# Kernel optimization log

Measured on AMD Instinct MI355X. Metric: run time of the kernel, lower is better.

## Reference

```python
import jax, jax.numpy as jnp
import numpy as np

B, L = 1, 8
K = 1024  # number of learned offsets / gathered channels
FULL_RES = (32, 32, 32)
EPS = 1e-5


def _trilinear(vol, cx, cy, cz):
    """torch.grid_sample (5D, mode='bilinear', padding='zeros', align_corners=False).
    vol: (D,H,W); cx,cy,cz: arbitrary matching shapes, normalized coords in [-1,1]
    with x->W, y->H, z->D (torch convention)."""
    D, H, W = vol.shape
    vflat = vol.reshape(-1)
    ix = ((cx + 1.0) * W - 1.0) * 0.5
    iy = ((cy + 1.0) * H - 1.0) * 0.5
    iz = ((cz + 1.0) * D - 1.0) * 0.5
    x0f, y0f, z0f = jnp.floor(ix), jnp.floor(iy), jnp.floor(iz)
    fx, fy, fz = ix - x0f, iy - y0f, iz - z0f
    x0 = x0f.astype(jnp.int32)
    y0 = y0f.astype(jnp.int32)
    z0 = z0f.astype(jnp.int32)
    out = jnp.zeros_like(ix)
    for dz in (0, 1):
        wz = fz if dz else 1.0 - fz
        zi = z0 + dz
        for dy in (0, 1):
            wy = fy if dy else 1.0 - fy
            yi = y0 + dy
            for dx in (0, 1):
                wx = fx if dx else 1.0 - fx
                xi = x0 + dx
                valid = (xi >= 0) & (xi < W) & (yi >= 0) & (yi < H) & (zi >= 0) & (zi < D)
                idx = (jnp.clip(zi, 0, D - 1) * H + jnp.clip(yi, 0, H - 1)) * W + jnp.clip(xi, 0, W - 1)
                out = out + (wz * wy * wx) * jnp.where(valid, vflat[idx], 0.0)
    return out


def _affine_identity_grid(D, H, W):
    # F.affine_grid(eye(3,4), align_corners=False): voxel-center coords in [-1,1]
    xs = (2.0 * jnp.arange(W) + 1.0) / W - 1.0
    ys = (2.0 * jnp.arange(H) + 1.0) / H - 1.0
    zs = (2.0 * jnp.arange(D) + 1.0) / D - 1.0
    zg, yg, xg = jnp.meshgrid(zs, ys, xs, indexing="ij")
    return jnp.stack([xg, yg, zg], axis=-1).reshape(-1, 3)  # (D*H*W, 3), order (x,y,z)


def _bn(x, g, b):
    # training-mode BatchNorm3d on flattened-spatial layout x:(B,C,N)
    m = jnp.mean(x, axis=(0, 2), keepdims=True)
    v = jnp.var(x, axis=(0, 2), keepdims=True)
    return (x - m) * jax.lax.rsqrt(v + EPS) * g[None, :, None] + b[None, :, None]


def _lin(x, w):  # 1x1x1 Conv3d, no bias: x:(B,C,N), w:(O,C)
    return jnp.einsum("bcn,oc->bon", x, w)


def _forward(images, offset1, w1, g1, b1, w2, g2, b2,
             w3a, w3b, w3c, w3d, g3a, b3a, g3b, b3b, g3c, b3c, g3d, b3d, w4, b4):
    Bn, _, D, H, W = images.shape
    base = _affine_identity_grid(D, H, W)  # (N,3)
    vols = images[:, 0]  # (B,D,H,W)

    def gather(off):  # off:(K,3) -> (B,K,N)
        c = base[None, :, :] + off[:, None, :]  # (K,N,3)
        return jax.vmap(lambda v: _trilinear(v, c[..., 0], c[..., 1], c[..., 2]))(vols)

    # dual offset trilinear gathers, subtracted (Obelisk feature)
    x = gather(offset1[:, 0]) - gather(offset1[:, 1])  # (B,1024,N)

    # grouped 1x1 conv (groups=4): (B,4,256,N) x (4,64,256) -> (B,256,N)
    xg = x.reshape(Bn, 4, 256, -1)
    y = jnp.einsum("bgcn,goc->bgon", xg, w1).reshape(Bn, 256, -1)
    x1 = jax.nn.relu(_bn(y, g1, b1))
    x2 = _bn(_lin(x1, w2), g2, b2)
    x3a = jnp.concatenate([x2, jax.nn.relu(_lin(x2, w3a))], axis=1)
    x3b = jnp.concatenate([x3a, jax.nn.relu(_lin(_bn(x3a, g3a, b3a), w3b))], axis=1)
    x3c = jnp.concatenate([x3b, jax.nn.relu(_lin(_bn(x3b, g3b, b3b), w3c))], axis=1)
    x3d = jnp.concatenate([x3c, jax.nn.relu(_lin(_bn(x3c, g3c, b3c), w3d))], axis=1)
    x4 = _lin(_bn(x3d, g3d, b3d), w4) + b4[None, :, None]
    out = jax.nn.sigmoid(x4)
    # F.interpolate to full_res is an identity here (grid already at full res)
    return out.reshape(Bn, -1, D, H, W)


def setup_inputs() -> dict:
    key = jax.random.key(0)
    ks = jax.random.split(key, 16)
    D, H, W = FULL_RES
    f32 = jnp.float32
    inp = {
        "images": jax.random.normal(ks[0], (B, 1, D, H, W), f32),
        "offset1": jax.random.normal(ks[1], (K, 2, 3), f32) * 0.2,
        "w1": jax.random.normal(ks[2], (4, 64, 256), f32) * 0.05,
        "g1": jnp.ones((256,), f32), "b1": jnp.zeros((256,), f32),
        "w2": jax.random.normal(ks[3], (128, 256), f32) * 0.05,
        "g2": jnp.ones((128,), f32), "b2": jnp.zeros((128,), f32),
        "w3a": jax.random.normal(ks[4], (32, 128), f32) * 0.05,
        "w3b": jax.random.normal(ks[5], (32, 160), f32) * 0.05,
        "w3c": jax.random.normal(ks[6], (32, 192), f32) * 0.05,
        "w3d": jax.random.normal(ks[7], (32, 224), f32) * 0.05,
        "g3a": jnp.ones((160,), f32), "b3a": jnp.zeros((160,), f32),
        "g3b": jnp.ones((192,), f32), "b3b": jnp.zeros((192,), f32),
        "g3c": jnp.ones((224,), f32), "b3c": jnp.zeros((224,), f32),
        "g3d": jnp.ones((256,), f32), "b3d": jnp.zeros((256,), f32),
        "w4": jax.random.normal(ks[8], (L, 256), f32) * 0.05,
        "b4": jnp.zeros((L,), f32),
    }
    return inp


def reference(images, offset1, w1, g1, b1, w2, g2, b2,
              w3a, w3b, w3c, w3d, g3a, b3a, g3b, b3b, g3c, b3c, g3d, b3d, w4, b4):
    return _forward(images, offset1, w1, g1, b1, w2, g2, b2,
                    w3a, w3b, w3c, w3d, g3a, b3a, g3b, b3b, g3c, b3c, g3d, b3d, w4, b4)
```

## Files before the change

### kernel.cpp

```cpp
#include <hip/hip_runtime.h>
#include <math.h>

#define VOXN 32768

typedef __attribute__((ext_vector_type(8))) short bf16x8;
typedef __attribute__((ext_vector_type(4))) float f32x4;

constexpr int OFF_STATS_Y   = 0;
constexpr int OFF_STATS_X2P = 512;
constexpr int OFF_STATS_H   = 768;
constexpr int OFF_TPAR      = 1280;
constexpr int OFF_W1A       = 17664;
constexpr int OFF_W2A       = 83200;
constexpr int OFF_W3AT      = 115968;
constexpr int OFF_W3BT      = 120064;
constexpr int OFF_W3CT      = 125184;
constexpr int OFF_W3DT      = 131328;
constexpr int OFF_W4T       = 138496;
constexpr int OFF_YH        = 140544;
constexpr int OFF_C0A       = OFF_YH;
constexpr int OFF_PERM      = OFF_YH + 1024;
constexpr int OFF_X2P       = 8529152;
constexpr int OFF_PVOLB     = OFF_X2P;

#define FMA4(A, W, X) { (A).x = fmaf((W).x, (X), (A).x); (A).y = fmaf((W).y, (X), (A).y); \
                        (A).z = fmaf((W).z, (X), (A).z); (A).w = fmaf((W).w, (X), (A).w); }
#define RELU4(A) { (A).x = fmaxf((A).x, 0.f); (A).y = fmaxf((A).y, 0.f); \
                   (A).z = fmaxf((A).z, 0.f); (A).w = fmaxf((A).w, 0.f); }
#define ZERO4(A) float4 A; (A).x = 0.f; (A).y = 0.f; (A).z = 0.f; (A).w = 0.f;

#define BFLY(s, q) { s += __shfl_xor(s, 32, 64); q += __shfl_xor(q, 32, 64); \
                     s += __shfl_xor(s, 16, 64); q += __shfl_xor(q, 16, 64); \
                     s += __shfl_xor(s,  8, 64); q += __shfl_xor(q,  8, 64); \
                     s += __shfl_xor(s,  4, 64); q += __shfl_xor(q,  4, 64); \
                     s += __shfl_xor(s,  2, 64); q += __shfl_xor(q,  2, 64); \
                     s += __shfl_xor(s,  1, 64); q += __shfl_xor(q,  1, 64); }
#define STASH1(V, O) { float s_ = (V), q_ = (V) * (V); BFLY(s_, q_) \
                       if (lane == (O)) { ms = s_; mq = q_; } }
#define STASH4(A, O0) STASH1((A).x, (O0)+0) STASH1((A).y, (O0)+1) \
                      STASH1((A).z, (O0)+2) STASH1((A).w, (O0)+3)

__device__ __forceinline__ unsigned short f2bf(float f) {
  unsigned int u = __float_as_uint(f);
  u += 0x7FFFu + ((u >> 16) & 1u);
  return (unsigned short)(u >> 16);
}

__device__ __forceinline__ float corner(const float* __restrict__ im, int x, int y, int z) {
  if (x >= 33 && x < 65 && y >= 33 && y < 65 && z >= 33 && z < 65)
    return im[((z - 33) * 32 + (y - 33)) * 32 + (x - 33)];
  return 0.f;
}

__device__ __forceinline__ int tap_c0(const float* __restrict__ offset1, int k, int s) {
  float ox = fminf(fmaxf(offset1[k * 6 + s * 3 + 0] * 16.f, -1000.f), 1000.f);
  float oy = fminf(fmaxf(offset1[k * 6 + s * 3 + 1] * 16.f, -1000.f), 1000.f);
  float oz = fminf(fmaxf(offset1[k * 6 + s * 3 + 2] * 16.f, -1000.f), 1000.f);
  int sx = (int)floorf(ox), sy = (int)floorf(oy), sz = (int)floorf(oz);
  bool valid = (sx >= -33 && sx <= 32) && (sy >= -33 && sy <= 32) && (sz >= -33 && sz <= 32);
  if (!valid) { sx = sy = sz = 0; }
  return (sz + 33) * 9604 + (sy + 33) * 98 + (sx + 33);
}

__global__ void s0a_setup(const float* __restrict__ images, const float* __restrict__ offset1,
                          const float* __restrict__ w3a, const float* __restrict__ w3b,
                          const float* __restrict__ w3c, const float* __restrict__ w3d,
                          const float* __restrict__ w4, float* __restrict__ ws)
{
  const int idx = blockIdx.x * blockDim.x + threadIdx.x;
  const int stride = gridDim.x * blockDim.x;
  for (int i = idx; i < 1280; i += stride) ws[i] = 0.f;
  uint4* qq = (uint4*)(ws + OFF_PVOLB);
  for (int i = idx; i < 941192; i += stride) {
    int x = i % 98, t = i / 98, y = t % 98, z = t / 98;
    uint4 f; f.x = 0u; f.y = 0u; f.z = 0u; f.w = 0u;
    if (x >= 32 && x <= 64 && y >= 32 && y <= 64 && z >= 32 && z <= 64) {
      float c000 = corner(images, x, y, z),     c100 = corner(images, x+1, y, z);
      float c010 = corner(images, x, y+1, z),   c110 = corner(images, x+1, y+1, z);
      float c001 = corner(images, x, y, z+1),   c101 = corner(images, x+1, y, z+1);
      float c011 = corner(images, x, y+1, z+1), c111 = corner(images, x+1, y+1, z+1);
      f.x = (unsigned int)f2bf(c000) | ((unsigned int)f2bf(c100) << 16);
      f.y = (unsigned int)f2bf(c010) | ((unsigned int)f2bf(c110) << 16);
      f.z = (unsigned int)f2bf(c001) | ((unsigned int)f2bf(c101) << 16);
      f.w = (unsigned int)f2bf(c011) | ((unsigned int)f2bf(c111) << 16);
    }
    qq[i] = f;
  }
  int* c0a = (int*)(ws + OFF_C0A);
  for (int k = idx; k < 1024; k += stride) c0a[k] = tap_c0(offset1, k, 0);
  for (int i = idx; i < 4096;  i += stride) { int o = i & 31,  c = i >> 5; ws[OFF_W3AT + i] = w3a[o * 128 + c]; }
  for (int i = idx; i < 5120;  i += stride) { int o = i & 31,  c = i >> 5; ws[OFF_W3BT + i] = w3b[o * 160 + c]; }
  for (int i = idx; i < 6144;  i += stride) { int o = i & 31,  c = i >> 5; ws[OFF_W3CT + i] = w3c[o * 192 + c]; }
  for (int i = idx; i < 7168;  i += stride) { int o = i & 31,  c = i >> 5; ws[OFF_W3DT + i] = w3d[o * 224 + c]; }
  for (int i = idx; i < 2048;  i += stride) { int l = i & 7,   c = i >> 3; ws[OFF_W4T + i] = w4[l * 256 + c]; }
}

__global__ void s0b_rank(float* __restrict__ ws)
{
  const int idx = blockIdx.x * blockDim.x + threadIdx.x;
  if (idx >= 1024) return;
  const int g = idx >> 8, k = idx & 255;
  const int* c0a = (const int*)(ws + OFF_C0A);
  int* perm = (int*)(ws + OFF_PERM);
  const int my = c0a[g * 256 + k];
  int rank = 0;
  for (int j = 0; j < 256; ++j) {
    int cj = c0a[g * 256 + j];
    rank += (cj < my) || (cj == my && j < k);
  }
  perm[g * 256 + rank] = k;
}

__global__ void s0c_build(const float* __restrict__ offset1, const float* __restrict__ w1,
                          const float* __restrict__ w2, float* __restrict__ ws)
{
  const int idx = blockIdx.x * blockDim.x + threadIdx.x;
  const int stride = gridDim.x * blockDim.x;
  const int* perm = (const int*)(ws + OFF_PERM);
  for (int p = idx; p < 1024; p += stride) {
    const int g = p >> 8;
    const int k = g * 256 + perm[p];
    float* tp = ws + OFF_TPAR + p * 16;
    for (int s = 0; s < 2; ++s) {
      float ox = fminf(fmaxf(offset1[k * 6 + s * 3 + 0] * 16.f, -1000.f), 1000.f);
      float oy = fminf(fmaxf(offset1[k * 6 + s * 3 + 1] * 16.f, -1000.f), 1000.f);
      float oz = fminf(fmaxf(offset1[k * 6 + s * 3 + 2] * 16.f, -1000.f), 1000.f);
      float fxf = floorf(ox), fyf = floorf(oy), fzf = floorf(oz);
      float fx = ox - fxf, fy = oy - fyf, fz = oz - fzf;
      int sx = (int)fxf, sy = (int)fyf, sz = (int)fzf;
      bool valid = (sx >= -33 && sx <= 32) && (sy >= -33 && sy <= 32) && (sz >= -33 && sz <= 32);
      if (!valid) { sx = sy = sz = 0; }
      float vm = valid ? 1.f : 0.f;
      int c0 = (sz + 33) * 9604 + (sy + 33) * 98 + (sx + 33);
      float sgn = s ? -1.f : 1.f;
      float wy0 = 1.f - fy, wy1 = fy, wz0 = 1.f - fz, wz1 = fz;
      tp[s * 8 + 0] = __int_as_float(c0);
      tp[s * 8 + 1] = vm * (1.f - fx);
      tp[s * 8 + 2] = vm * fx;
      tp[s * 8 + 3] = vm * sgn * wz0 * wy0;
      tp[s * 8 + 4] = vm * sgn * wz0 * wy1;
      tp[s * 8 + 5] = vm * sgn * wz1 * wy0;
      tp[s * 8 + 6] = vm * sgn * wz1 * wy1;
      tp[s * 8 + 7] = 0.f;
    }
  }
  for (int i = idx; i < 32768; i += stride) {
    int jp = i & 3;
    int l  = (i >> 2) & 63;
    int ks = (i >> 8) & 7;
    int mt = (i >> 11) & 3;
    int g  = i >> 13;
    int row = mt * 16 + (l & 15);
    int kbase = g * 256 + ks * 32 + (l >> 4) * 8 + jp * 2;
    int ka = perm[kbase], kb = perm[kbase + 1];
    unsigned short b0 = f2bf(w1[g * 16384 + row * 256 + ka]);
    unsigned short b1 = f2bf(w1[g * 16384 + row * 256 + kb]);
    ws[OFF_W1A + i] = __uint_as_float((unsigned int)b0 | ((unsigned int)b1 << 16));
  }
  for (int i = idx; i < 16384; i += stride) {
    int jp = i & 3;
    int l  = (i >> 2) & 63;
    int ks = (i >> 8) & 7;
    int mt = i >> 11;
    int row = mt * 16 + (l & 15);
    int k = ks * 32 + (l >> 4) * 8 + jp * 2;
    unsigned short b0 = f2bf(w2[row * 256 + k]);
    unsigned short b1 = f2bf(w2[row * 256 + k + 1]);
    ws[OFF_W2A + i] = __uint_as_float((unsigned int)b0 | ((unsigned int)b1 << 16));
  }
}

__device__ __forceinline__ float tapB(const uint4* __restrict__ Q, int vbase,
                                      const float4 t0, const float4 t1)
{
  uint4 c = Q[vbase + __float_as_int(t0.x)];
  float c0 = __uint_as_float(c.x << 16), c1 = __uint_as_float(c.x & 0xffff0000u);
  float c2 = __uint_as_float(c.y << 16), c3 = __uint_as_float(c.y & 0xffff0000u);
  float c4 = __uint_as_float(c.z << 16), c5 = __uint_as_float(c.z & 0xffff0000u);
  float c6 = __uint_as_float(c.w << 16), c7 = __uint_as_float(c.w & 0xffff0000u);
  float h0 = c0 * t0.y + c1 * t0.z;
  float h1 = c2 * t0.y + c3 * t0.z;
  float h2 = c4 * t0.y + c5 * t0.z;
  float h3 = c6 * t0.y + c7 * t0.z;
  return h0 * t0.w + h1 * t1.x + h2 * t1.y + h3 * t1.z;
}

__global__ __launch_bounds__(256, 4) void s1_gather_gemm(
    const uint4* __restrict__ pvolB, const float* __restrict__ tparP,
    const float4* __restrict__ apack, float* __restrict__ y, float* __restrict__ stats_y)
{
  __shared__ unsigned short xt[128 * 72];
  const int tid = threadIdx.x;
  const int lane = tid & 63;
  const int wv = tid >> 6;
  const int g = blockIdx.y;
  const int v0 = blockIdx.x * 128;
  const int n = tid & 127;
  const int khalf = tid >> 7;
  const int v = v0 + n;
  const int vbase = (v >> 10) * 9604 + ((v >> 5) & 31) * 98 + (v & 31);
  const float4* tq_base = (const float4*)(tparP + g * 4096);

  f32x4 acc[8];
  #pragma unroll
  for (int i = 0; i < 8; ++i) acc[i] = (f32x4){0.f, 0.f, 0.f, 0.f};

  for (int ch = 0; ch < 4; ++ch) {
    const int kb = ch * 64 + khalf * 32;
    __syncthreads();
    #pragma unroll 2
    for (int i2 = 0; i2 < 32; i2 += 2) {
      const int kt = kb + i2;
      float4 t0 = tq_base[kt*4+0], t1 = tq_base[kt*4+1];
      float4 t2 = tq_base[kt*4+2], t3 = tq_base[kt*4+3];
      float xv0 = tapB(pvolB, vbase, t0, t1) + tapB(pvolB, vbase, t2, t3);
      float4 u0 = tq_base[kt*4+4], u1 = tq_base[kt*4+5];
      float4 u2 = tq_base[kt*4+6], u3 = tq_base[kt*4+7];
      float xv1 = tapB(pvolB, vbase, u0, u1) + tapB(pvolB, vbase, u2, u3);
      unsigned int pk = (unsigned int)f2bf(xv0) | ((unsigned int)f2bf(xv1) << 16);
      *(unsigned int*)&xt[n * 72 + khalf * 32 + i2] = pk;
    }
    __syncthreads();
    #pragma unroll
    for (int s = 0; s < 2; ++s) {
      float4 araw = apack[(((g * 4 + wv) * 8) + ch * 2 + s) * 64 + lane];
      bf16x8 a = *reinterpret_cast<bf16x8*>(&araw);
      #pragma unroll
      for (int nt = 0; nt < 8; ++nt) {
        const unsigned short* bp = &xt[(nt * 16 + (lane & 15)) * 72 + s * 32 + (lane >> 4) * 8];
        float4 braw = *(const float4*)bp;
        bf16x8 b = *reinterpret_cast<bf16x8*>(&braw);
        acc[nt] = __builtin_amdgcn_mfma_f32_16x16x32_bf16(a, b, acc[nt], 0, 0, 0);
      }
    }
  }
  const int obase = g << 6;
  float srow0 = 0.f, srow1 = 0.f, srow2 = 0.f, srow3 = 0.f;
  float qrow0 = 0.f, qrow1 = 0.f, qrow2 = 0.f, qrow3 = 0.f;
  #pragma unroll
  for (int nt = 0; nt < 8; ++nt) {
    const int col = v0 + nt * 16 + (lane & 15);
    const int rbase = obase + wv * 16 + (lane >> 4) * 4;
    float e0 = acc[nt][0], e1 = acc[nt][1], e2 = acc[nt][2], e3 = acc[nt][3];
    y[(size_t)(rbase + 0) * VOXN + col] = e0;
    y[(size_t)(rbase + 1) * VOXN + col] = e1;
    y[(size_t)(rbase + 2) * VOXN + col] = e2;
    y[(size_t)(rbase + 3) * VOXN + col] = e3;
    srow0 += e0; qrow0 += e0 * e0;
    srow1 += e1; qrow1 += e1 * e1;
    srow2 += e2; qrow2 += e2 * e2;
    srow3 += e3; qrow3 += e3 * e3;
  }
  #define ROWRED(S, Q, R) { \
    float s_ = S, q_ = Q; \
    s_ += __shfl_xor(s_, 1, 64); q_ += __shfl_xor(q_, 1, 64); \
    s_ += __shfl_xor(s_, 2, 64); q_ += __shfl_xor(q_, 2, 64); \
    s_ += __shfl_xor(s_, 4, 64); q_ += __shfl_xor(q_, 4, 64); \
    s_ += __shfl_xor(s_, 8, 64); q_ += __shfl_xor(q_, 8, 64); \
    if ((lane & 15) == 0) { \
      int row = obase + wv * 16 + (lane >> 4) * 4 + (R); \
      atomicAdd(&stats_y[row], s_); atomicAdd(&stats_y[256 + row], q_); } }
  ROWRED(srow0, qrow0, 0) ROWRED(srow1, qrow1, 1)
  ROWRED(srow2, qrow2, 2) ROWRED(srow3, qrow3, 3)
  #undef ROWRED
}

__global__ __launch_bounds__(256) void s2_bn_gemm(
    const float* __restrict__ y, const float* __restrict__ stats_y,
    const float* __restrict__ g1, const float* __restrict__ b1,
    const float4* __restrict__ w2a, float* __restrict__ x2p, float* __restrict__ stats_x2p)
{
  __shared__ float As[256], Bs[256];
  __shared__ unsigned short xt[128 * 72];
  const int tid = threadIdx.x;
  const int lane = tid & 63;
  const int wv = tid >> 6;
  const int n = tid & 127;
  const int khalf = tid >> 7;
  const int half = blockIdx.y;
  const int v0 = blockIdx.x * 128;
  const int v = v0 + n;
  {
    float m = stats_y[tid] * (1.f / VOXN);
    float vv = stats_y[256 + tid] * (1.f / VOXN) - m * m;
    float a = g1[tid] * rsqrtf(vv + 1e-5f);
    As[tid] = a; Bs[tid] = b1[tid] - m * a;
  }
  f32x4 acc[8];
  #pragma unroll
  for (int i = 0; i < 8; ++i) acc[i] = (f32x4){0.f, 0.f, 0.f, 0.f};

  for (int ch = 0; ch < 4; ++ch) {
    const int kb = ch * 64 + khalf * 32;
    __syncthreads();
    #pragma unroll 2
    for (int i2 = 0; i2 < 32; i2 += 2) {
      const int c = kb + i2;
      float t0 = fmaxf(fmaf(y[(size_t)c * VOXN + v], As[c], Bs[c]), 0.f);
      float t1 = fmaxf(fmaf(y[(size_t)(c + 1) * VOXN + v], As[c + 1], Bs[c + 1]), 0.f);
      unsigned int pk = (unsigned int)f2bf(t0) | ((unsigned int)f2bf(t1) << 16);
      *(unsigned int*)&xt[n * 72 + khalf * 32 + i2] = pk;
    }
    __syncthreads();
    #pragma unroll
    for (int s = 0; s < 2; ++s) {
      float4 araw = w2a[(((half * 4 + wv) * 8) + ch * 2 + s) * 64 + lane];
      bf16x8 a = *reinterpret_cast<bf16x8*>(&araw);
      #pragma unroll
      for (int nt = 0; nt < 8; ++nt) {
        const unsigned short* bp = &xt[(nt * 16 + (lane & 15)) * 72 + s * 32 + (lane >> 4) * 8];
        float4 braw = *(const float4*)bp;
        bf16x8 b = *reinterpret_cast<bf16x8*>(&braw);
        acc[nt] = __builtin_amdgcn_mfma_f32_16x16x32_bf16(a, b, acc[nt], 0, 0, 0);
      }
    }
  }
  const int mbase = half * 64 + wv * 16;
  float srow0 = 0.f, srow1 = 0.f, srow2 = 0.f, srow3 = 0.f;
  float qrow0 = 0.f, qrow1 = 0.f, qrow2 = 0.f, qrow3 = 0.f;
  #pragma unroll
  for (int nt = 0; nt < 8; ++nt) {
    const int col = v0 + nt * 16 + (lane & 15);
    const int rbase = mbase + (lane >> 4) * 4;
    float e0 = acc[nt][0], e1 = acc[nt][1], e2 = acc[nt][2], e3 = acc[nt][3];
    x2p[(size_t)(rbase + 0) * VOXN + col] = e0;
    x2p[(size_t)(rbase + 1) * VOXN + col] = e1;
    x2p[(size_t)(rbase + 2) * VOXN + col] = e2;
    x2p[(size_t)(rbase + 3) * VOXN + col] = e3;
    srow0 += e0; qrow0 += e0 * e0;
    srow1 += e1; qrow1 += e1 * e1;
    srow2 += e2; qrow2 += e2 * e2;
    srow3 += e3; qrow3 += e3 * e3;
  }
  #define ROWRED2(S, Q, R) { \
    float s_ = S, q_ = Q; \
    s_ += __shfl_xor(s_, 1, 64); q_ += __shfl_xor(q_, 1, 64); \
    s_ += __shfl_xor(s_, 2, 64); q_ += __shfl_xor(q_, 2, 64); \
    s_ += __shfl_xor(s_, 4, 64); q_ += __shfl_xor(q_, 4, 64); \
    s_ += __shfl_xor(s_, 8, 64); q_ += __shfl_xor(q_, 8, 64); \
    if ((lane & 15) == 0) { \
      int row = mbase + (lane >> 4) * 4 + (R); \
      atomicAdd(&stats_x2p[row], s_); atomicAdd(&stats_x2p[128 + row], q_); } }
  ROWRED2(srow0, qrow0, 0) ROWRED2(srow1, qrow1, 1)
  ROWRED2(srow2, qrow2, 2) ROWRED2(srow3, qrow3, 3)
  #undef ROWRED2
}

__device__ __forceinline__ void x2_coef(const float* __restrict__ stats_x2p,
                                        const float* __restrict__ g2, const float* __restrict__ b2,
                                        int c, float& a2, float& b2c, float& mx, float& vx)
{
  float m2 = stats_x2p[c] * (1.f / VOXN);
  float v2 = stats_x2p[128 + c] * (1.f / VOXN) - m2 * m2;
  a2 = g2[c] * rsqrtf(v2 + 1e-5f);
  b2c = b2[c] - m2 * a2;
  mx = b2[c];
  vx = a2 * a2 * v2;
}

__global__ __launch_bounds__(256) void s3_ha(
    const float* __restrict__ x2p, const float* __restrict__ stats_x2p,
    const float* __restrict__ g2, const float* __restrict__ b2,
    const float* __restrict__ w3at, float* __restrict__ H, float* __restrict__ stats_H)
{
  __shared__ float As[128], Bs[128];
  __shared__ float redS[4][4], redQ[4][4];
  const int tid = threadIdx.x;
  const int lane = tid & 63;
  const int wv = tid >> 6;
  if (tid < 128) {
    float a2, b2c, mx, vx;
    x2_coef(stats_x2p, g2, b2, tid, a2, b2c, mx, vx);
    As[tid] = a2; Bs[tid] = b2c;
  }
  __syncthreads();
  const int qh = blockIdx.y;
  const int n = blockIdx.x * 256 + tid;
  ZERO4(a0)
  #pragma unroll 8
  for (int c = 0; c < 128; ++c) {
    float x2v = fmaf(x2p[(size_t)c * VOXN + n], As[c], Bs[c]);
    const float4* wk = (const float4*)(w3at + c * 32 + qh * 4);
    float4 w = wk[0];
    FMA4(a0, w, x2v)
  }
  RELU4(a0)
  const int ob = 128 + qh * 4;
  H[((size_t)(ob + 0)) * VOXN + n] = a0.x;
  H[((size_t)(ob + 1)) * VOXN + n] = a0.y;
  H[((size_t)(ob + 2)) * VOXN + n] = a0.z;
  H[((size_t)(ob + 3)) * VOXN + n] = a0.w;
  float ms = 0.f, mq = 0.f;
  STASH4(a0, 0)
  if (lane < 4) { redS[wv][lane] = ms; redQ[wv][lane] = mq; }
  __syncthreads();
  if (tid < 4) {
    float s = redS[0][tid] + redS[1][tid] + redS[2][tid] + redS[3][tid];
    float qq = redQ[0][tid] + redQ[1][tid] + redQ[2][tid] + redQ[3][tid];
    atomicAdd(&stats_H[ob + tid], s);
    atomicAdd(&stats_H[256 + ob + tid], qq);
  }
}

template<int CIN>
__global__ __launch_bounds__(256) void s_dense(
    const float* __restrict__ x2p, const float* __restrict__ stats_x2p,
    const float* __restrict__ g2, const float* __restrict__ b2,
    const float* __restrict__ Hin, const float* __restrict__ stats_H,
    const float* __restrict__ g, const float* __restrict__ b,
    const float* __restrict__ wt, float* __restrict__ H, float* __restrict__ stats_out, int och)
{
  __shared__ float As[CIN], Bs[CIN];
  __shared__ float redS[4][4], redQ[4][4];
  const int tid = threadIdx.x;
  const int lane = tid & 63;
  const int wv = tid >> 6;
  if (tid < 128) {
    float a2, b2c, mx, vx;
    x2_coef(stats_x2p, g2, b2, tid, a2, b2c, mx, vx);
    float A = g[tid] * rsqrtf(vx + 1e-5f);
    float B = b[tid] - mx * A;
    As[tid] = A * a2; Bs[tid] = fmaf(A, b2c, B);
  } else if (tid < CIN) {
    float m = stats_H[tid] * (1.f / VOXN);
    float vv = stats_H[256 + tid] * (1.f / VOXN) - m * m;
    float A = g[tid] * rsqrtf(vv + 1e-5f);
    As[tid] = A; Bs[tid] = b[tid] - m * A;
  }
  __syncthreads();
  const int osub = blockIdx.y * 4;
  const int n = blockIdx.x * 256 + tid;
  ZERO4(a0)
  #pragma unroll 8
  for (int c = 0; c < 128; ++c) {
    float t = fmaf(x2p[(size_t)c * VOXN + n], As[c], Bs[c]);
    const float4* wk = (const float4*)(wt + c * 32 + osub);
    float4 w = wk[0];
    FMA4(a0, w, t)
  }
  #pragma unroll 8
  for (int c = 128; c < CIN; ++c) {
    float t = fmaf(Hin[(size_t)c * VOXN + n], As[c], Bs[c]);
    const float4* wk = (const float4*)(wt + c * 32 + osub);
    float4 w = wk[0];
    FMA4(a0, w, t)
  }
  RELU4(a0)
  const int ob = och + osub;
  H[((size_t)(ob + 0)) * VOXN + n] = a0.x;
  H[((size_t)(ob + 1)) * VOXN + n] = a0.y;
  H[((size_t)(ob + 2)) * VOXN + n] = a0.z;
  H[((size_t)(ob + 3)) * VOXN + n] = a0.w;
  float ms = 0.f, mq = 0.f;
  STASH4(a0, 0)
  if (lane < 4) { redS[wv][lane] = ms; redQ[wv][lane] = mq; }
  __syncthreads();
  if (tid < 4) {
    float s = redS[0][tid] + redS[1][tid] + redS[2][tid] + redS[3][tid];
    float qq = redQ[0][tid] + redQ[1][tid] + redQ[2][tid] + redQ[3][tid];
    atomicAdd(&stats_out[ob + tid], s);
    atomicAdd(&stats_out[256 + ob + tid], qq);
  }
}

__global__ __launch_bounds__(256) void s7_final(
    const float* __restrict__ x2p, const float* __restrict__ stats_x2p,
    const float* __restrict__ g2, const float* __restrict__ b2,
    const float* __restrict__ H, const float* __restrict__ stats_H,
    const float* __restrict__ g3d, const float* __restrict__ b3d,
    const float* __restrict__ w4t, const float* __restrict__ b4, float* __restrict__ out)
{
  __shared__ float As[256], Bs[256];
  __shared__ float part[3][64][8];
  const int tid = threadIdx.x;
  const int vox = tid & 63;
  const int cq = tid >> 6;
  const int n = blockIdx.x * 64 + vox;
  if (tid < 128) {
    float a2, b2c, mx, vx;
    x2_coef(stats_x2p, g2, b2, tid, a2, b2c, mx, vx);
    float A = g3d[tid] * rsqrtf(vx + 1e-5f);
    float B = b3d[tid] - mx * A;
    As[tid] = A * a2; Bs[tid] = fmaf(A, b2c, B);
  } else {
    float m = stats_H[tid] * (1.f / VOXN);
    float vv = stats_H[256 + tid] * (1.f / VOXN) - m * m;
    float A = g3d[tid] * rsqrtf(vv + 1e-5f);
    As[tid] = A; Bs[tid] = b3d[tid] - m * A;
  }
  __syncthreads();
  ZERO4(a0) ZERO4(a1)
  const int c0 = cq * 64;
  #pragma unroll 8
  for (int c = c0; c < c0 + 64; ++c) {
    const float* src = (c < 128) ? x2p : (H - (size_t)0);
    float t = fmaf(src[(size_t)c * VOXN + n], As[c], Bs[c]);
    const float4* wk = (const float4*)(w4t + c * 8);
    float4 w;
    w = wk[0]; FMA4(a0, w, t)
    w = wk[1]; FMA4(a1, w, t)
  }
  if (cq > 0) {
    part[cq - 1][vox][0] = a0.x; part[cq - 1][vox][1] = a0.y;
    part[cq - 1][vox][2] = a0.z; part[cq - 1][vox][3] = a0.w;
    part[cq - 1][vox][4] = a1.x; part[cq - 1][vox][5] = a1.y;
    part[cq - 1][vox][6] = a1.z; part[cq - 1][vox][7] = a1.w;
  }
  __syncthreads();
  if (cq == 0) {
    float r0 = a0.x + part[0][vox][0] + part[1][vox][0] + part[2][vox][0];
    float r1 = a0.y + part[0][vox][1] + part[1][vox][1] + part[2][vox][1];
    float r2 = a0.z + part[0][vox][2] + part[1][vox][2] + part[2][vox][2];
    float r3 = a0.w + part[0][vox][3] + part[1][vox][3] + part[2][vox][3];
    float r4 = a1.x + part[0][vox][4] + part[1][vox][4] + part[2][vox][4];
    float r5 = a1.y + part[0][vox][5] + part[1][vox][5] + part[2][vox][5];
    float r6 = a1.z + part[0][vox][6] + part[1][vox][6] + part[2][vox][6];
    float r7 = a1.w + part[0][vox][7] + part[1][vox][7] + part[2][vox][7];
    out[(size_t)0 * VOXN + n] = 1.f / (1.f + expf(-(r0 + b4[0])));
    out[(size_t)1 * VOXN + n] = 1.f / (1.f + expf(-(r1 + b4[1])));
    out[(size_t)2 * VOXN + n] = 1.f / (1.f + expf(-(r2 + b4[2])));
    out[(size_t)3 * VOXN + n] = 1.f / (1.f + expf(-(r3 + b4[3])));
    out[(size_t)4 * VOXN + n] = 1.f / (1.f + expf(-(r4 + b4[4])));
    out[(size_t)5 * VOXN + n] = 1.f / (1.f + expf(-(r5 + b4[5])));
    out[(size_t)6 * VOXN + n] = 1.f / (1.f + expf(-(r6 + b4[6])));
    out[(size_t)7 * VOXN + n] = 1.f / (1.f + expf(-(r7 + b4[7])));
  }
}

extern "C" void kernel_launch(void* const* d_in, const int* in_sizes, int n_in,
                              void* d_out, int out_size, void* d_ws, size_t ws_size,
                              hipStream_t stream)
{
  const float* images  = (const float*)d_in[0];
  const float* offset1 = (const float*)d_in[1];
  const float* w1  = (const float*)d_in[2];
  const float* g1  = (const float*)d_in[3];
  const float* b1  = (const float*)d_in[4];
  const float* w2  = (const float*)d_in[5];
  const float* g2  = (const float*)d_in[6];
  const float* b2  = (const float*)d_in[7];
  const float* w3a = (const float*)d_in[8];
  const float* w3b = (const float*)d_in[9];
  const float* w3c = (const float*)d_in[10];
  const float* w3d = (const float*)d_in[11];
  const float* g3a = (const float*)d_in[12];
  const float* b3a = (const float*)d_in[13];
  const float* g3b = (const float*)d_in[14];
  const float* b3b = (const float*)d_in[15];
  const float* g3c = (const float*)d_in[16];
  const float* b3c = (const float*)d_in[17];
  const float* g3d = (const float*)d_in[18];
  const float* b3d = (const float*)d_in[19];
  const float* w4  = (const float*)d_in[20];
  const float* b4  = (const float*)d_in[21];

  float* ws  = (float*)d_ws;
  float* out = (float*)d_out;

  float* statsY = ws + OFF_STATS_Y;
  float* statsX = ws + OFF_STATS_X2P;
  float* statsH = ws + OFF_STATS_H;
  float* YH     = ws + OFF_YH;
  float* x2p    = ws + OFF_X2P;

  s0a_setup<<<dim3(256), dim3(256), 0, stream>>>(images, offset1, w3a, w3b, w3c, w3d, w4, ws);
  s0b_rank<<<dim3(4), dim3(256), 0, stream>>>(ws);
  s0c_build<<<dim3(64), dim3(256), 0, stream>>>(offset1, w1, w2, ws);
  s1_gather_gemm<<<dim3(256, 4), dim3(256), 0, stream>>>(
      (const uint4*)(ws + OFF_PVOLB), ws + OFF_TPAR,
      (const float4*)(ws + OFF_W1A), YH, statsY);
  s2_bn_gemm<<<dim3(256, 2), dim3(256), 0, stream>>>(
      YH, statsY, g1, b1, (const float4*)(ws + OFF_W2A), x2p, statsX);
  s3_ha<<<dim3(128, 8), dim3(256), 0, stream>>>(x2p, statsX, g2, b2, ws + OFF_W3AT, YH, statsH);
  s_dense<160><<<dim3(128, 8), dim3(256), 0, stream>>>(
      x2p, statsX, g2, b2, YH, statsH, g3a, b3a, ws + OFF_W3BT, YH, statsH, 160);
  s_dense<192><<<dim3(128, 8), dim3(256), 0, stream>>>(
      x2p, statsX, g2, b2, YH, statsH, g3b, b3b, ws + OFF_W3CT, YH, statsH, 192);
  s_dense<224><<<dim3(128, 8), dim3(256), 0, stream>>>(
      x2p, statsX, g2, b2, YH, statsH, g3c, b3c, ws + OFF_W3DT, YH, statsH, 224);
  s7_final<<<dim3(512), dim3(256), 0, stream>>>(
      x2p, statsX, g2, b2, YH, statsH, g3d, b3d, ws + OFF_W4T, b4, out);
}
```

Before: 312.0 us.

## Run dense-block 1x1 convs on bf16 MFMA with shared-memory staged activations

New measurement: 449.6 us. 44.1% more time.

```diff
diff --git a/kernel.cpp b/kernel.cpp
--- a/kernel.cpp
+++ b/kernel.cpp
@@ -12,10 +12,10 @@
 constexpr int OFF_TPAR      = 1280;
 constexpr int OFF_W1A       = 17664;
 constexpr int OFF_W2A       = 83200;
-constexpr int OFF_W3AT      = 115968;
-constexpr int OFF_W3BT      = 120064;
-constexpr int OFF_W3CT      = 125184;
-constexpr int OFF_W3DT      = 131328;
+constexpr int OFF_W3AP      = 115968;
+constexpr int OFF_W3BP      = 120064;
+constexpr int OFF_W3CP      = 125184;
+constexpr int OFF_W3DP      = 131328;
 constexpr int OFF_W4T       = 138496;
 constexpr int OFF_YH        = 140544;
 constexpr int OFF_C0A       = OFF_YH;
@@ -25,20 +25,7 @@
 
 #define FMA4(A, W, X) { (A).x = fmaf((W).x, (X), (A).x); (A).y = fmaf((W).y, (X), (A).y); \
                         (A).z = fmaf((W).z, (X), (A).z); (A).w = fmaf((W).w, (X), (A).w); }
-#define RELU4(A) { (A).x = fmaxf((A).x, 0.f); (A).y = fmaxf((A).y, 0.f); \
-                   (A).z = fmaxf((A).z, 0.f); (A).w = fmaxf((A).w, 0.f); }
 #define ZERO4(A) float4 A; (A).x = 0.f; (A).y = 0.f; (A).z = 0.f; (A).w = 0.f;
-
-#define BFLY(s, q) { s += __shfl_xor(s, 32, 64); q += __shfl_xor(q, 32, 64); \
-                     s += __shfl_xor(s, 16, 64); q += __shfl_xor(q, 16, 64); \
-                     s += __shfl_xor(s,  8, 64); q += __shfl_xor(q,  8, 64); \
-                     s += __shfl_xor(s,  4, 64); q += __shfl_xor(q,  4, 64); \
-                     s += __shfl_xor(s,  2, 64); q += __shfl_xor(q,  2, 64); \
-                     s += __shfl_xor(s,  1, 64); q += __shfl_xor(q,  1, 64); }
-#define STASH1(V, O) { float s_ = (V), q_ = (V) * (V); BFLY(s_, q_) \
-                       if (lane == (O)) { ms = s_; mq = q_; } }
-#define STASH4(A, O0) STASH1((A).x, (O0)+0) STASH1((A).y, (O0)+1) \
-                      STASH1((A).z, (O0)+2) STASH1((A).w, (O0)+3)
 
 __device__ __forceinline__ unsigned short f2bf(float f) {
   unsigned int u = __float_as_uint(f);
@@ -63,8 +50,6 @@
 }
 
 __global__ void s0a_setup(const float* __restrict__ images, const float* __restrict__ offset1,
-                          const float* __restrict__ w3a, const float* __restrict__ w3b,
-                          const float* __restrict__ w3c, const float* __restrict__ w3d,
                           const float* __restrict__ w4, float* __restrict__ ws)
 {
   const int idx = blockIdx.x * blockDim.x + threadIdx.x;
@@ -88,11 +73,7 @@
   }
   int* c0a = (int*)(ws + OFF_C0A);
   for (int k = idx; k < 1024; k += stride) c0a[k] = tap_c0(offset1, k, 0);
-  for (int i = idx; i < 4096;  i += stride) { int o = i & 31,  c = i >> 5; ws[OFF_W3AT + i] = w3a[o * 128 + c]; }
-  for (int i = idx; i < 5120;  i += stride) { int o = i & 31,  c = i >> 5; ws[OFF_W3BT + i] = w3b[o * 160 + c]; }
-  for (int i = idx; i < 6144;  i += stride) { int o = i & 31,  c = i >> 5; ws[OFF_W3CT + i] = w3c[o * 192 + c]; }
-  for (int i = idx; i < 7168;  i += stride) { int o = i & 31,  c = i >> 5; ws[OFF_W3DT + i] = w3d[o * 224 + c]; }
-  for (int i = idx; i < 2048;  i += stride) { int l = i & 7,   c = i >> 3; ws[OFF_W4T + i] = w4[l * 256 + c]; }
+  for (int i = idx; i < 2048;  i += stride) { int l = i & 7, c = i >> 3; ws[OFF_W4T + i] = w4[l * 256 + c]; }
 }
 
 __global__ void s0b_rank(float* __restrict__ ws)
@@ -112,7 +93,10 @@
 }
 
 __global__ void s0c_build(const float* __restrict__ offset1, const float* __restrict__ w1,
-                          const float* __restrict__ w2, float* __restrict__ ws)
+                          const float* __restrict__ w2,
+                          const float* __restrict__ w3a, const float* __restrict__ w3b,
+                          const float* __restrict__ w3c, const float* __restrict__ w3d,
+                          float* __restrict__ ws)
 {
   const int idx = blockIdx.x * blockDim.x + threadIdx.x;
   const int stride = gridDim.x * blockDim.x;
@@ -168,6 +152,50 @@
     unsigned short b1 = f2bf(w2[row * 256 + k + 1]);
     ws[OFF_W2A + i] = __uint_as_float((unsigned int)b0 | ((unsigned int)b1 << 16));
   }
+  for (int i = idx; i < 2048; i += stride) {
+    int jp = i & 3, l = (i >> 2) & 63, rest = i >> 8;
+    int ks = rest & 3, mt = rest >> 2;
+    int row = mt * 16 + (l & 15);
+    int k = ks * 32 + (l >> 4) * 8 + jp * 2;
+    unsigned short b0 = f2bf(w3a[row * 128 + k]);
+    unsigned short b1 = f2bf(w3a[row * 128 + k + 1]);
+    ws[OFF_W3AP + i] = __uint_as_float((unsigned int)b0 | ((unsigned int)b1 << 16));
+  }
+  for (int i = idx; i < 3072; i += stride) {
+    int jp = i & 3, l = (i >> 2) & 63, rest = i >> 8;
+    int ks = rest % 6, mt = rest / 6;
+    int row = mt * 16 + (l & 15);
+    int k = ks * 32 + (l >> 4) * 8 + jp * 2;
+    unsigned int pk = 0u;
+    if (k < 160) {
+      unsigned short b0 = f2bf(w3b[row * 160 + k]);
+      unsigned short b1 = f2bf(w3b[row * 160 + k + 1]);
+      pk = (unsigned int)b0 | ((unsigned int)b1 << 16);
+    }
+    ws[OFF_W3BP + i] = __uint_as_float(pk);
+  }
+  for (int i = idx; i < 3072; i += stride) {
+    int jp = i & 3, l = (i >> 2) & 63, rest = i >> 8;
+    int ks = rest % 6, mt = rest / 6;
+    int row = mt * 16 + (l & 15);
+    int k = ks * 32 + (l >> 4) * 8 + jp * 2;
+    unsigned short b0 = f2bf(w3c[row * 192 + k]);
+    unsigned short b1 = f2bf(w3c[row * 192 + k + 1]);
+    ws[OFF_W3CP + i] = __uint_as_float((unsigned int)b0 | ((unsigned int)b1 << 16));
+  }
+  for (int i = idx; i < 4096; i += stride) {
+    int jp = i & 3, l = (i >> 2) & 63, rest = i >> 8;
+    int ks = rest & 7, mt = rest >> 3;
+    int row = mt * 16 + (l & 15);
+    int k = ks * 32 + (l >> 4) * 8 + jp * 2;
+    unsigned int pk = 0u;
+    if (k < 224) {
+      unsigned short b0 = f2bf(w3d[row * 224 + k]);
+      unsigned short b1 = f2bf(w3d[row * 224 + k + 1]);
+      pk = (unsigned int)b0 | ((unsigned int)b1 << 16);
+    }
+    ws[OFF_W3DP + i] = __uint_as_float(pk);
+  }
 }
 
 __device__ __forceinline__ float tapB(const uint4* __restrict__ Q, int vbase,
@@ -358,109 +386,117 @@
   vx = a2 * a2 * v2;
 }
 
-__global__ __launch_bounds__(256) void s3_ha(
+template<int CIN, int NCH, bool FUSE>
+__global__ __launch_bounds__(512) void sd_mfma(
     const float* __restrict__ x2p, const float* __restrict__ stats_x2p,
     const float* __restrict__ g2, const float* __restrict__ b2,
-    const float* __restrict__ w3at, float* __restrict__ H, float* __restrict__ stats_H)
-{
-  __shared__ float As[128], Bs[128];
-  __shared__ float redS[4][4], redQ[4][4];
+    const float* __restrict__ Hbase, const float* __restrict__ stats_H,
+    const float* __restrict__ g, const float* __restrict__ b,
+    const float4* __restrict__ wpack, float* __restrict__ Hout,
+    float* __restrict__ stats_out, int och)
+{
+  __shared__ float As[256], Bs[256];
+  __shared__ unsigned short xt[128 * 72];
   const int tid = threadIdx.x;
   const int lane = tid & 63;
   const int wv = tid >> 6;
+  const int mt = wv & 1;
+  const int nq = wv >> 1;
+  const int n = tid & 127;
+  const int kq = (tid >> 7) & 3;
+  const int v0 = blockIdx.x * 128;
+  const int v = v0 + n;
+
   if (tid < 128) {
     float a2, b2c, mx, vx;
     x2_coef(stats_x2p, g2, b2, tid, a2, b2c, mx, vx);
-    As[tid] = a2; Bs[tid] = b2c;
-  }
-  __syncthreads();
-  const int qh = blockIdx.y;
-  const int n = blockIdx.x * 256 + tid;
-  ZERO4(a0)
-  #pragma unroll 8
-  for (int c = 0; c < 128; ++c) {
-    float x2v = fmaf(x2p[(size_t)c * VOXN + n], As[c], Bs[c]);
-    const float4* wk = (const float4*)(w3at + c * 32 + qh * 4);
-    float4 w = wk[0];
-    FMA4(a0, w, x2v)
-  }
-  RELU4(a0)
-  const int ob = 128 + qh * 4;
-  H[((size_t)(ob + 0)) * VOXN + n] = a0.x;
-  H[((size_t)(ob + 1)) * VOXN + n] = a0.y;
-  H[((size_t)(ob + 2)) * VOXN + n] = a0.z;
-  H[((size_t)(ob + 3)) * VOXN + n] = a0.w;
-  float ms = 0.f, mq = 0.f;
-  STASH4(a0, 0)
-  if (lane < 4) { redS[wv][lane] = ms; redQ[wv][lane] = mq; }
-  __syncthreads();
-  if (tid < 4) {
-    float s = redS[0][tid] + redS[1][tid] + redS[2][tid] + redS[3][tid];
-    float qq = redQ[0][tid] + redQ[1][tid] + redQ[2][tid] + redQ[3][tid];
-    atomicAdd(&stats_H[ob + tid], s);
-    atomicAdd(&stats_H[256 + ob + tid], qq);
-  }
-}
-
-template<int CIN>
-__global__ __launch_bounds__(256) void s_dense(
-    const float* __restrict__ x2p, const float* __restrict__ stats_x2p,
-    const float* __restrict__ g2, const float* __restrict__ b2,
-    const float* __restrict__ Hin, const float* __restrict__ stats_H,
-    const float* __restrict__ g, const float* __restrict__ b,
-    const float* __restrict__ wt, float* __restrict__ H, float* __restrict__ stats_out, int och)
-{
-  __shared__ float As[CIN], Bs[CIN];
-  __shared__ float redS[4][4], redQ[4][4];
-  const int tid = threadIdx.x;
-  const int lane = tid & 63;
-  const int wv = tid >> 6;
-  if (tid < 128) {
-    float a2, b2c, mx, vx;
-    x2_coef(stats_x2p, g2, b2, tid, a2, b2c, mx, vx);
-    float A = g[tid] * rsqrtf(vx + 1e-5f);
-    float B = b[tid] - mx * A;
-    As[tid] = A * a2; Bs[tid] = fmaf(A, b2c, B);
+    if (FUSE) {
+      float A = g[tid] * rsqrtf(vx + 1e-5f);
+      float B = b[tid] - mx * A;
+      As[tid] = A * a2; Bs[tid] = fmaf(A, b2c, B);
+    } else {
+      As[tid] = a2; Bs[tid] = b2c;
+    }
   } else if (tid < CIN) {
     float m = stats_H[tid] * (1.f / VOXN);
     float vv = stats_H[256 + tid] * (1.f / VOXN) - m * m;
     float A = g[tid] * rsqrtf(vv + 1e-5f);
     As[tid] = A; Bs[tid] = b[tid] - m * A;
-  }
-  __syncthreads();
-  const int osub = blockIdx.y * 4;
-  const int n = blockIdx.x * 256 + tid;
-  ZERO4(a0)
-  #pragma unroll 8
-  for (int c = 0; c < 128; ++c) {
-    float t = fmaf(x2p[(size_t)c * VOXN + n], As[c], Bs[c]);
-    const float4* wk = (const float4*)(wt + c * 32 + osub);
-    float4 w = wk[0];
-    FMA4(a0, w, t)
-  }
-  #pragma unroll 8
-  for (int c = 128; c < CIN; ++c) {
-    float t = fmaf(Hin[(size_t)c * VOXN + n], As[c], Bs[c]);
-    const float4* wk = (const float4*)(wt + c * 32 + osub);
-    float4 w = wk[0];
-    FMA4(a0, w, t)
-  }
-  RELU4(a0)
-  const int ob = och + osub;
-  H[((size_t)(ob + 0)) * VOXN + n] = a0.x;
-  H[((size_t)(ob + 1)) * VOXN + n] = a0.y;
-  H[((size_t)(ob + 2)) * VOXN + n] = a0.z;
-  H[((size_t)(ob + 3)) * VOXN + n] = a0.w;
-  float ms = 0.f, mq = 0.f;
-  STASH4(a0, 0)
-  if (lane < 4) { redS[wv][lane] = ms; redQ[wv][lane] = mq; }
-  __syncthreads();
-  if (tid < 4) {
-    float s = redS[0][tid] + redS[1][tid] + redS[2][tid] + redS[3][tid];
-    float qq = redQ[0][tid] + redQ[1][tid] + redQ[2][tid] + redQ[3][tid];
-    atomicAdd(&stats_out[ob + tid], s);
-    atomicAdd(&stats_out[256 + ob + tid], qq);
-  }
+  } else if (tid < 256) {
+    As[tid] = 0.f; Bs[tid] = 0.f;
+  }
+
+  f32x4 acc0 = (f32x4){0.f,0.f,0.f,0.f}, acc1 = (f32x4){0.f,0.f,0.f,0.f};
+
+  #pragma unroll
+  for (int ch = 0; ch < NCH; ++ch) {
+    __syncthreads();
+    const float* src = (ch < 2) ? x2p : Hbase;
+    #pragma unroll
+    for (int i2 = 0; i2 < 16; i2 += 2) {
+      int c = ch * 64 + kq * 16 + i2;
+      float t0 = fmaf(src[(size_t)c * VOXN + v], As[c], Bs[c]);
+      float t1 = fmaf(src[(size_t)(c + 1) * VOXN + v], As[c + 1], Bs[c + 1]);
+      unsigned int pk = (unsigned int)f2bf(t0) | ((unsigned int)f2bf(t1) << 16);
+      *(unsigned int*)&xt[n * 72 + kq * 16 + i2] = pk;
+    }
+    __syncthreads();
+    #pragma unroll
+    for (int s = 0; s < 2; ++s) {
+      float4 araw = wpack[(mt * (2 * NCH) + ch * 2 + s) * 64 + lane];
+      bf16x8 a = *reinterpret_cast<bf16x8*>(&araw);
+      {
+        const int nt = nq * 2;
+        const unsigned short* bp = &xt[(nt * 16 + (lane & 15)) * 72 + s * 32 + (lane >> 4) * 8];
+        float4 braw = *(const float4*)bp;
+        bf16x8 bb = *reinterpret_cast<bf16x8*>(&braw);
+        acc0 = __builtin_amdgcn_mfma_f32_16x16x32_bf16(a, bb, acc0, 0, 0, 0);
+      }
+      {
+        const int nt = nq * 2 + 1;
+        const unsigned short* bp = &xt[(nt * 16 + (lane & 15)) * 72 + s * 32 + (lane >> 4) * 8];
+        float4 braw = *(const float4*)bp;
+        bf16x8 bb = *reinterpret_cast<bf16x8*>(&braw);
+        acc1 = __builtin_amdgcn_mfma_f32_16x16x32_bf16(a, bb, acc1, 0, 0, 0);
+      }
+    }
+  }
+  const int rbase = och + mt * 16 + (lane >> 4) * 4;
+  float sr0, sr1, sr2, sr3, qr0, qr1, qr2, qr3;
+  {
+    const int col = v0 + (nq * 2) * 16 + (lane & 15);
+    float e0 = fmaxf(acc0[0], 0.f), e1 = fmaxf(acc0[1], 0.f);
+    float e2 = fmaxf(acc0[2], 0.f), e3 = fmaxf(acc0[3], 0.f);
+    Hout[(size_t)(rbase + 0) * VOXN + col] = e0;
+    Hout[(size_t)(rbase + 1) * VOXN + col] = e1;
+    Hout[(size_t)(rbase + 2) * VOXN + col] = e2;
+    Hout[(size_t)(rbase + 3) * VOXN + col] = e3;
+    sr0 = e0; qr0 = e0 * e0; sr1 = e1; qr1 = e1 * e1;
+    sr2 = e2; qr2 = e2 * e2; sr3 = e3; qr3 = e3 * e3;
+  }
+  {
+    const int col = v0 + (nq * 2 + 1) * 16 + (lane & 15);
+    float e0 = fmaxf(acc1[0], 0.f), e1 = fmaxf(acc1[1], 0.f);
+    float e2 = fmaxf(acc1[2], 0.f), e3 = fmaxf(acc1[3], 0.f);
+    Hout[(size_t)(rbase + 0) * VOXN + col] = e0;
+    Hout[(size_t)(rbase + 1) * VOXN + col] = e1;
+    Hout[(size_t)(rbase + 2) * VOXN + col] = e2;
+    Hout[(size_t)(rbase + 3) * VOXN + col] = e3;
+    sr0 += e0; qr0 += e0 * e0; sr1 += e1; qr1 += e1 * e1;
+    sr2 += e2; qr2 += e2 * e2; sr3 += e3; qr3 += e3 * e3;
+  }
+  #define ROWRED3(S, Q, R) { \
+    float s_ = S, q_ = Q; \
+    s_ += __shfl_xor(s_, 1, 64); q_ += __shfl_xor(q_, 1, 64); \
+    s_ += __shfl_xor(s_, 2, 64); q_ += __shfl_xor(q_, 2, 64); \
+    s_ += __shfl_xor(s_, 4, 64); q_ += __shfl_xor(q_, 4, 64); \
+    s_ += __shfl_xor(s_, 8, 64); q_ += __shfl_xor(q_, 8, 64); \
+    if ((lane & 15) == 0) { \
+      int row = rbase + (R); \
+      atomicAdd(&stats_out[row], s_); atomicAdd(&stats_out[256 + row], q_); } }
+  ROWRED3(sr0, qr0, 0) ROWRED3(sr1, qr1, 1)
+  ROWRED3(sr2, qr2, 2) ROWRED3(sr3, qr3, 3)
+  #undef ROWRED3
 }
 
 __global__ __launch_bounds__(256) void s7_final(
@@ -493,7 +529,7 @@
   const int c0 = cq * 64;
   #pragma unroll 8
   for (int c = c0; c < c0 + 64; ++c) {
-    const float* src = (c < 128) ? x2p : (H - (size_t)0);
+    const float* src = (c < 128) ? x2p : H;
     float t = fmaf(src[(size_t)c * VOXN + n], As[c], Bs[c]);
     const float4* wk = (const float4*)(w4t + c * 8);
     float4 w;
@@ -563,21 +599,26 @@
   float* YH     = ws + OFF_YH;
   float* x2p    = ws + OFF_X2P;
 
-  s0a_setup<<<dim3(256), dim3(256), 0, stream>>>(images, offset1, w3a, w3b, w3c, w3d, w4, ws);
+  s0a_setup<<<dim3(256), dim3(256), 0, stream>>>(images, offset1, w4, ws);
   s0b_rank<<<dim3(4), dim3(256), 0, stream>>>(ws);
-  s0c_build<<<dim3(64), dim3(256), 0, stream>>>(offset1, w1, w2, ws);
+  s0c_build<<<dim3(64), dim3(256), 0, stream>>>(offset1, w1, w2, w3a, w3b, w3c, w3d, ws);
   s1_gather_gemm<<<dim3(256, 4), dim3(256), 0, stream>>>(
       (const uint4*)(ws + OFF_PVOLB), ws + OFF_TPAR,
       (const float4*)(ws + OFF_W1A), YH, statsY);
   s2_bn_gemm<<<dim3(256, 2), dim3(256), 0, stream>>>(
       YH, statsY, g1, b1, (const float4*)(ws + OFF_W2A), x2p, statsX);
-  s3_ha<<<dim3(128, 8), dim3(256), 0, stream>>>(x2p, statsX, g2, b2, ws + OFF_W3AT, YH, statsH);
-  s_dense<160><<<dim3(128, 8), dim3(256), 0, stream>>>(
-      x2p, statsX, g2, b2, YH, statsH, g3a, b3a, ws + OFF_W3BT, YH, statsH, 160);
-  s_dense<192><<<dim3(128, 8), dim3(256), 0, stream>>>(
-      x2p, statsX, g2, b2, YH, statsH, g3b, b3b, ws + OFF_W3CT, YH, statsH, 192);
-  s_dense<224><<<dim3(128, 8), dim3(256), 0, stream>>>(
-      x2p, statsX, g2, b2, YH, statsH, g3c, b3c, ws + OFF_W3DT, YH, statsH, 224);
+  sd_mfma<128, 2, false><<<dim3(256), dim3(512), 0, stream>>>(
+      x2p, statsX, g2, b2, YH, statsH, g2, b2,
+      (const float4*)(ws + OFF_W3AP), YH, statsH, 128);
+  sd_mfma<160, 3, true><<<dim3(256), dim3(512), 0, stream>>>(
+      x2p, statsX, g2, b2, YH, statsH, g3a, b3a,
+      (const float4*)(ws + OFF_W3BP), YH, statsH, 160);
+  sd_mfma<192, 3, true><<<dim3(256), dim3(512), 0, stream>>>(
+      x2p, statsX, g2, b2, YH, statsH, g3b, b3b,
+      (const float4*)(ws + OFF_W3CP), YH, statsH, 192);
+  sd_mfma<224, 4, true><<<dim3(256), dim3(512), 0, stream>>>(
+      x2p, statsX, g2, b2, YH, statsH, g3c, b3c,
+      (const float4*)(ws + OFF_W3DP), YH, statsH, 224);
   s7_final<<<dim3(512), dim3(256), 0, stream>>>(
       x2p, statsX, g2, b2, YH, statsH, g3d, b3d, ws + OFF_W4T, b4, out);
 }
```
